# Kernel optimization log

Measured on AMD Instinct MI355X. Metric: run time of the kernel, lower is better.

The kernel has to match this reference:

```python
import jax, jax.numpy as jnp
import numpy as np

B, N, E, H = 16, 512, 256, 8
ALPHA = 0.2  # leaky relu negative slope


def setup_inputs() -> dict:
    key = jax.random.key(0)
    k1, k2, k3, k4, k5, k6 = jax.random.split(key, 6)
    x = jax.random.normal(k1, (B, N, E), dtype=jnp.float32)
    A = (jax.random.uniform(k2, (B, N, N)) < 0.3).astype(jnp.float32)
    s = 1.0 / np.sqrt(E)
    W = jax.random.uniform(k3, (E, E), minval=-s, maxval=s, dtype=jnp.float32)
    bW = jax.random.uniform(k4, (E,), minval=-s, maxval=s, dtype=jnp.float32)
    a = jax.random.uniform(k5, (E, 2 * H), minval=-s, maxval=s, dtype=jnp.float32)
    ba = jax.random.uniform(k6, (2 * H,), minval=-s, maxval=s, dtype=jnp.float32)
    return {"x": x, "A": A, "W": W, "bW": bW, "a": a, "ba": ba}


def reference(x, A, W, bW, a, ba):
    # Wh = W(x): [B, N, E]
    Wh = jnp.einsum("bne,ef->bnf", x, W) + bW
    # attention coefficients: a(Wh) -> [B, N, 2H] -> [B, H, N, 2]
    e12 = (jnp.einsum("bne,eh->bnh", Wh, a) + ba).reshape(B, N, H, 2).transpose(0, 2, 1, 3)
    e = e12[..., 0:1] + jnp.swapaxes(e12[..., 1:2], -2, -1)  # [B, H, N, N]
    # split heads: [B, H, N, D]
    Whh = Wh.reshape(B, N, H, E // H).transpose(0, 2, 1, 3)
    mask = A[:, None, :, :] > 0.5  # [B, H(bcast), N, N]
    neg = jnp.finfo(e.dtype).min
    score = jnp.where(mask, jax.nn.leaky_relu(e, ALPHA), neg)
    att = jax.nn.softmax(score, axis=-1)
    # rows with no neighbors: torch softmax(-inf row) -> nan -> nan_to_num -> 0
    has_nbr = jnp.any(mask, axis=-1, keepdims=True)
    att = jnp.where(has_nbr, att, 0.0)
    out = jnp.einsum("bhij,bhjd->bhid", att, Whh)  # [B, H, N, D]
    out = out.transpose(0, 2, 1, 3).reshape(B, N, E)
    # dropout is identity in eval/reference mode
    return jax.nn.relu(out)
```

## Files before the change

kernel.cpp:

```cpp
#include <hip/hip_runtime.h>
#include <math.h>

#define Bv 16
#define Nv 512
#define Ev 256
#define Hv 8
#define Dv 32
#define LOG2E 1.44269504088896340736f

typedef _Float16 half8 __attribute__((ext_vector_type(8)));
typedef _Float16 half4_t __attribute__((ext_vector_type(4)));
typedef float f32x4 __attribute__((ext_vector_type(4)));

__global__ __launch_bounds__(256) void fused_pre(const float* __restrict__ x,
                                                 const float* __restrict__ W,
                                                 const float* __restrict__ bW,
                                                 const float* __restrict__ aP,
                                                 const float* __restrict__ ba,
                                                 const float* __restrict__ A,
                                                 _Float16* __restrict__ WhT,
                                                 float* __restrict__ Wa,
                                                 float* __restrict__ cba,
                                                 unsigned int* __restrict__ Abm) {
    __shared__ _Float16 Wp[64][264];
    __shared__ _Float16 xs[64][40];
    __shared__ _Float16 ldsTr[64][72];

    const int tid = threadIdx.x;
    const int blk = blockIdx.x;

    if (blk < 512) {
        const int m0 = (blk >> 2) * 64;
        const int n0 = (blk & 3) * 64;
        const int w = tid >> 6;
        const int lane = tid & 63;
        const int row = lane & 15;
        const int strip = lane >> 4;

        {
            const float* wrow = &W[(size_t)tid * Ev + n0];
            #pragma unroll
            for (int u = 0; u < 16; ++u) {
                float4 v = *(const float4*)&wrow[u * 4];
                Wp[u * 4 + 0][tid] = (_Float16)v.x;
                Wp[u * 4 + 1][tid] = (_Float16)v.y;
                Wp[u * 4 + 2][tid] = (_Float16)v.z;
                Wp[u * 4 + 3][tid] = (_Float16)v.w;
            }
        }

        f32x4 acc[4] = {{0.f, 0.f, 0.f, 0.f}, {0.f, 0.f, 0.f, 0.f},
                        {0.f, 0.f, 0.f, 0.f}, {0.f, 0.f, 0.f, 0.f}};
        const int sr = tid >> 2;
        const int skg = (tid & 3) * 8;

        for (int k0 = 0; k0 < Ev; k0 += 32) {
            {
                const float* xp = &x[(size_t)(m0 + sr) * Ev + k0 + skg];
                float4 v0 = *(const float4*)xp;
                float4 v1 = *(const float4*)(xp + 4);
                half8 hv;
                hv[0] = (_Float16)v0.x; hv[1] = (_Float16)v0.y;
                hv[2] = (_Float16)v0.z; hv[3] = (_Float16)v0.w;
                hv[4] = (_Float16)v1.x; hv[5] = (_Float16)v1.y;
                hv[6] = (_Float16)v1.z; hv[7] = (_Float16)v1.w;
                *(half8*)&xs[sr][skg] = hv;
            }
            __syncthreads();

            half8 af = *(const half8*)&xs[w * 16 + row][strip * 8];
            #pragma unroll
            for (int ns = 0; ns < 4; ++ns) {
                half8 bf = *(const half8*)&Wp[ns * 16 + row][k0 + strip * 8];
                acc[ns] = __builtin_amdgcn_mfma_f32_16x16x32_f16(af, bf, acc[ns], 0, 0, 0);
            }
            __syncthreads();
        }

        #pragma unroll
        for (int ns = 0; ns < 4; ++ns) {
            const float bias = bW[n0 + ns * 16 + row];
            half4_t hv;
            hv[0] = (_Float16)(acc[ns][0] + bias);
            hv[1] = (_Float16)(acc[ns][1] + bias);
            hv[2] = (_Float16)(acc[ns][2] + bias);
            hv[3] = (_Float16)(acc[ns][3] + bias);
            *(half4_t*)&ldsTr[ns * 16 + row][w * 16 + strip * 4] = hv;
        }
        __syncthreads();

        {
            const int n = tid >> 2, jg = tid & 3;
            uint4 v0 = *(const uint4*)&ldsTr[n][jg * 16];
            uint4 v1 = *(const uint4*)&ldsTr[n][jg * 16 + 8];
            const int ng = n0 + n;
            const int h = ng >> 5, d = ng & 31;
            const int b = m0 >> 9, j0 = m0 & 511;
            _Float16* dst = &WhT[(((size_t)b * Hv + h) * Dv + d) * Nv + j0 + jg * 16];
            *(uint4*)dst = v0;
            *(uint4*)(dst + 8) = v1;
        }
    } else if (blk < 528) {
        const int e = (blk - 512) * 16 + (tid >> 4);
        const int c = tid & 15;
        float dot = 0.f;
        for (int k4 = 0; k4 < 64; ++k4) {
            float4 wv = *(const float4*)&W[(size_t)e * Ev + k4 * 4];
            dot += wv.x * aP[(k4 * 4 + 0) * 16 + c];
            dot += wv.y * aP[(k4 * 4 + 1) * 16 + c];
            dot += wv.z * aP[(k4 * 4 + 2) * 16 + c];
            dot += wv.w * aP[(k4 * 4 + 3) * 16 + c];
        }
        Wa[e * 16 + c] = dot;
    } else if (blk == 528) {
        if (tid < 16) {
            float d = ba[tid];
            for (int k = 0; k < Ev; ++k) d += bW[k] * aP[k * 16 + tid];
            cba[tid] = d;
        }
    } else {
        const int ablk = blk - 529;
        const int w = tid >> 6, lane = tid & 63;
        const size_t base = (size_t)ablk * 2048 + w * 512;
        #pragma unroll
        for (int r = 0; r < 8; ++r) {
            const size_t f = base + r * 64 + lane;
            const bool pred = A[f] > 0.5f;
            unsigned long long m = __ballot(pred);
            if (lane == 0) *(unsigned long long*)&Abm[f >> 5] = m;
        }
    }
}

__global__ __launch_bounds__(256) void e12_kernel(const float* __restrict__ x,
                                                  const float* __restrict__ Wa,
                                                  const float* __restrict__ cba,
                                                  float* __restrict__ e1,
                                                  float* __restrict__ e2) {
    __shared__ float WaS[Ev][16];
    __shared__ float cbaS[16];

    const int tid = threadIdx.x;
    const int m0 = blockIdx.x * 32;

    #pragma unroll
    for (int u = 0; u < 4; ++u) {
        int f = tid + u * 256;
        *(float4*)&WaS[f >> 2][(f & 3) * 4] = *(const float4*)&Wa[f * 4];
    }
    if (tid < 16) cbaS[tid] = cba[tid];
    __syncthreads();

    const int r = tid >> 3;
    const int q = (tid >> 1) & 3;
    const int kh = tid & 1;
    const int m = m0 + r;

    const float* xr = &x[(size_t)m * Ev + kh * 128];
    float4 acc = {0.f, 0.f, 0.f, 0.f};

    #pragma unroll 8
    for (int it = 0; it < 32; ++it) {
        float4 xv = *(const float4*)&xr[it * 4];
        const int kb = kh * 128 + it * 4;
        float4 w0 = *(const float4*)&WaS[kb + 0][q * 4];
        float4 w1 = *(const float4*)&WaS[kb + 1][q * 4];
        float4 w2 = *(const float4*)&WaS[kb + 2][q * 4];
        float4 w3 = *(const float4*)&WaS[kb + 3][q * 4];
        acc.x += xv.x * w0.x + xv.y * w1.x + xv.z * w2.x + xv.w * w3.x;
        acc.y += xv.x * w0.y + xv.y * w1.y + xv.z * w2.y + xv.w * w3.y;
        acc.z += xv.x * w0.z + xv.y * w1.z + xv.z * w2.z + xv.w * w3.z;
        acc.w += xv.x * w0.w + xv.y * w1.w + xv.z * w2.w + xv.w * w3.w;
    }

    acc.x += __shfl_xor(acc.x, 1);
    acc.y += __shfl_xor(acc.y, 1);
    acc.z += __shfl_xor(acc.z, 1);
    acc.w += __shfl_xor(acc.w, 1);

    if (kh == 0) {
        const int b = m >> 9, i = m & 511;
        #pragma unroll
        for (int cc = 0; cc < 4; ++cc) {
            const int c = q * 4 + cc;
            const float val = ((cc == 0) ? acc.x : (cc == 1) ? acc.y : (cc == 2) ? acc.z : acc.w)
                              + cbaS[c];
            const int h = c >> 1;
            float* dst = (c & 1) ? e2 : e1;
            dst[(((b << 3) + h) << 9) + i] = val;
        }
    }
}

__global__ __launch_bounds__(256) void attn_kernel(const unsigned int* __restrict__ Abm,
                                                   const _Float16* __restrict__ WhT,
                                                   const float* __restrict__ e1g,
                                                   const float* __restrict__ e2g,
                                                   float* __restrict__ out) {
    __shared__ _Float16 whT[Dv * Nv];
    __shared__ float E2pS[Nv];
    __shared__ float E2nS[Nv];

    const int tid = threadIdx.x;
    const int i0 = blockIdx.x * 128;
    const int h = blockIdx.y;
    const int b = blockIdx.z;
    const int bh = (b << 3) + h;

    const _Float16* src = WhT + (size_t)bh * (Dv * Nv);
    #pragma unroll
    for (int u = 0; u < 8; ++u) {
        int f = tid + u * 256;
        int d = f >> 6, bq = f & 63;
        uint4 v = *(const uint4*)(src + d * Nv + bq * 8);
        *(uint4*)&whT[d * Nv + ((bq ^ (d & 7)) * 8)] = v;
    }
    {
        float ea = e2g[(bh << 9) + tid] * LOG2E;
        E2pS[tid] = __builtin_amdgcn_exp2f(ea);
        E2nS[tid] = __builtin_amdgcn_exp2f(0.2f * ea);
        float eb = e2g[(bh << 9) + tid + 256] * LOG2E;
        E2pS[tid + 256] = __builtin_amdgcn_exp2f(eb);
        E2nS[tid + 256] = __builtin_amdgcn_exp2f(0.2f * eb);
    }
    __syncthreads();

    const int w = tid >> 6;
    const int lane = tid & 63;
    const int row = lane & 15;
    const int strip = lane >> 4;
    const int iA = i0 + (w << 5) + row;
    const int iB = iA + 16;

    const float e1A = e1g[(bh << 9) + iA] * LOG2E;
    const float e1B = e1g[(bh << 9) + iB] * LOG2E;
    const float E1pA = __builtin_amdgcn_exp2f(e1A);
    const float E1nA = __builtin_amdgcn_exp2f(0.2f * e1A);
    const float E1pB = __builtin_amdgcn_exp2f(e1B);
    const float E1nB = __builtin_amdgcn_exp2f(0.2f * e1B);

    const uint4* bpA = (const uint4*)&Abm[((size_t)b * Nv + iA) << 4];
    const uint4 mA0 = bpA[0], mA1 = bpA[1], mA2 = bpA[2], mA3 = bpA[3];
    const uint4* bpB = (const uint4*)&Abm[((size_t)b * Nv + iB) << 4];
    const uint4 mB0 = bpB[0], mB1 = bpB[1], mB2 = bpB[2], mB3 = bpB[3];

    const int sh = strip << 3;
    const int d0 = lane & 15;
    const int sw = d0 & 7;
    const _Float16* brow0 = &whT[d0 * Nv];
    const _Float16* brow1 = &whT[(16 + d0) * Nv];

    f32x4 accA0 = {0.f, 0.f, 0.f, 0.f}, accA1 = accA0;
    f32x4 accB0 = accA0, accB1 = accA0;
    float denA = 0.f, denB = 0.f;

    #pragma unroll
    for (int t = 0; t < 16; ++t) {
        const uint4 mqA = (t >> 2) == 0 ? mA0 : (t >> 2) == 1 ? mA1 : (t >> 2) == 2 ? mA2 : mA3;
        const uint4 mqB = (t >> 2) == 0 ? mB0 : (t >> 2) == 1 ? mB1 : (t >> 2) == 2 ? mB2 : mB3;
        const unsigned int dwA = (t & 3) == 0 ? mqA.x : (t & 3) == 1 ? mqA.y : (t & 3) == 2 ? mqA.z : mqA.w;
        const unsigned int dwB = (t & 3) == 0 ? mqB.x : (t & 3) == 1 ? mqB.y : (t & 3) == 2 ? mqB.z : mqB.w;
        const unsigned int byA = (dwA >> sh) & 0xFFu;
        const unsigned int byB = (dwB >> sh) & 0xFFu;

        const float4 p0 = *(const float4*)&E2pS[t * 32 + sh];
        const float4 p1 = *(const float4*)&E2pS[t * 32 + sh + 4];
        const float4 n0 = *(const float4*)&E2nS[t * 32 + sh];
        const float4 n1 = *(const float4*)&E2nS[t * 32 + sh + 4];

        const float qA0 = (byA & 1u)   ? fmaxf(E1pA * p0.x, E1nA * n0.x) : 0.f;
        const float qA1 = (byA & 2u)   ? fmaxf(E1pA * p0.y, E1nA * n0.y) : 0.f;
        const float qA2 = (byA & 4u)   ? fmaxf(E1pA * p0.z, E1nA * n0.z) : 0.f;
        const float qA3 = (byA & 8u)   ? fmaxf(E1pA * p0.w, E1nA * n0.w) : 0.f;
        const float qA4 = (byA & 16u)  ? fmaxf(E1pA * p1.x, E1nA * n1.x) : 0.f;
        const float qA5 = (byA & 32u)  ? fmaxf(E1pA * p1.y, E1nA * n1.y) : 0.f;
        const float qA6 = (byA & 64u)  ? fmaxf(E1pA * p1.z, E1nA * n1.z) : 0.f;
        const float qA7 = (byA & 128u) ? fmaxf(E1pA * p1.w, E1nA * n1.w) : 0.f;
        const float qB0 = (byB & 1u)   ? fmaxf(E1pB * p0.x, E1nB * n0.x) : 0.f;
        const float qB1 = (byB & 2u)   ? fmaxf(E1pB * p0.y, E1nB * n0.y) : 0.f;
        const float qB2 = (byB & 4u)   ? fmaxf(E1pB * p0.z, E1nB * n0.z) : 0.f;
        const float qB3 = (byB & 8u)   ? fmaxf(E1pB * p0.w, E1nB * n0.w) : 0.f;
        const float qB4 = (byB & 16u)  ? fmaxf(E1pB * p1.x, E1nB * n1.x) : 0.f;
        const float qB5 = (byB & 32u)  ? fmaxf(E1pB * p1.y, E1nB * n1.y) : 0.f;
        const float qB6 = (byB & 64u)  ? fmaxf(E1pB * p1.z, E1nB * n1.z) : 0.f;
        const float qB7 = (byB & 128u) ? fmaxf(E1pB * p1.w, E1nB * n1.w) : 0.f;

        denA += ((qA0 + qA1) + (qA2 + qA3)) + ((qA4 + qA5) + (qA6 + qA7));
        denB += ((qB0 + qB1) + (qB2 + qB3)) + ((qB4 + qB5) + (qB6 + qB7));

        half8 afA, afB;
        afA[0] = (_Float16)qA0; afA[1] = (_Float16)qA1;
        afA[2] = (_Float16)qA2; afA[3] = (_Float16)qA3;
        afA[4] = (_Float16)qA4; afA[5] = (_Float16)qA5;
        afA[6] = (_Float16)qA6; afA[7] = (_Float16)qA7;
        afB[0] = (_Float16)qB0; afB[1] = (_Float16)qB1;
        afB[2] = (_Float16)qB2; afB[3] = (_Float16)qB3;
        afB[4] = (_Float16)qB4; afB[5] = (_Float16)qB5;
        afB[6] = (_Float16)qB6; afB[7] = (_Float16)qB7;

        const int bq = ((t << 2) + strip) ^ sw;
        half8 b0 = *(const half8*)(brow0 + bq * 8);
        half8 b1 = *(const half8*)(brow1 + bq * 8);
        accA0 = __builtin_amdgcn_mfma_f32_16x16x32_f16(afA, b0, accA0, 0, 0, 0);
        accA1 = __builtin_amdgcn_mfma_f32_16x16x32_f16(afA, b1, accA1, 0, 0, 0);
        accB0 = __builtin_amdgcn_mfma_f32_16x16x32_f16(afB, b0, accB0, 0, 0, 0);
        accB1 = __builtin_amdgcn_mfma_f32_16x16x32_f16(afB, b1, accB1, 0, 0, 0);
    }

    denA += __shfl_xor(denA, 16);
    denA += __shfl_xor(denA, 32);
    denB += __shfl_xor(denB, 16);
    denB += __shfl_xor(denB, 32);

    #pragma unroll
    for (int e = 0; e < 4; ++e) {
        const float dnA = __shfl(denA, (strip << 2) + e);
        const float rvA = (dnA > 0.f) ? (1.f / dnA) : 0.f;
        const int orA = i0 + (w << 5) + (strip << 2) + e;
        float* opA = &out[((size_t)b * Nv + orA) * Ev + (h << 5)];
        opA[d0] = fmaxf(accA0[e] * rvA, 0.f);
        opA[16 + d0] = fmaxf(accA1[e] * rvA, 0.f);

        const float dnB = __shfl(denB, (strip << 2) + e);
        const float rvB = (dnB > 0.f) ? (1.f / dnB) : 0.f;
        const int orB = orA + 16;
        float* opB = &out[((size_t)b * Nv + orB) * Ev + (h << 5)];
        opB[d0] = fmaxf(accB0[e] * rvB, 0.f);
        opB[16 + d0] = fmaxf(accB1[e] * rvB, 0.f);
    }
}

extern "C" void kernel_launch(void* const* d_in, const int* in_sizes, int n_in,
                              void* d_out, int out_size, void* d_ws, size_t ws_size,
                              hipStream_t stream) {
    const float* x  = (const float*)d_in[0];
    const float* A  = (const float*)d_in[1];
    const float* W  = (const float*)d_in[2];
    const float* bW = (const float*)d_in[3];
    const float* a  = (const float*)d_in[4];
    const float* ba = (const float*)d_in[5];
    float* out = (float*)d_out;

    char* ws = (char*)d_ws;
    float*        Wa  = (float*)(ws);
    float*        cba = (float*)(ws + 16384);
    float*        e1  = (float*)(ws + 32768);
    float*        e2  = (float*)(ws + 294912);
    unsigned int* Abm = (unsigned int*)(ws + 557056);
    _Float16*     WhT = (_Float16*)(ws + 1572864);

    fused_pre<<<2577, 256, 0, stream>>>(x, W, bW, a, ba, A, WhT, Wa, cba, Abm);
    e12_kernel<<<dim3(Bv * Nv / 32), 256, 0, stream>>>(x, Wa, cba, e1, e2);
    attn_kernel<<<dim3(Nv / 128, Hv, Bv), 256, 0, stream>>>(Abm, WhT, e1, e2, out);
}
```

Baseline: 42.75 us.

## Use MFMA for attention logits, double-buffer x tile, pack fp16 converts

```diff
diff --git a/kernel.cpp b/kernel.cpp
--- a/kernel.cpp
+++ b/kernel.cpp
@@ -10,6 +10,7 @@
 
 typedef _Float16 half8 __attribute__((ext_vector_type(8)));
 typedef _Float16 half4_t __attribute__((ext_vector_type(4)));
+typedef __fp16 fp16x2 __attribute__((ext_vector_type(2)));
 typedef float f32x4 __attribute__((ext_vector_type(4)));
 
 __global__ __launch_bounds__(256) void fused_pre(const float* __restrict__ x,
@@ -19,11 +20,11 @@
                                                  const float* __restrict__ ba,
                                                  const float* __restrict__ A,
                                                  _Float16* __restrict__ WhT,
-                                                 float* __restrict__ Wa,
+                                                 _Float16* __restrict__ WaT,
                                                  float* __restrict__ cba,
                                                  unsigned int* __restrict__ Abm) {
     __shared__ _Float16 Wp[64][264];
-    __shared__ _Float16 xs[64][40];
+    __shared__ _Float16 xs[2][64][40];
     __shared__ _Float16 ldsTr[64][72];
 
     const int tid = threadIdx.x;
@@ -49,32 +50,51 @@
             }
         }
 
+        const int sr = tid >> 2;
+        const int skg = (tid & 3) * 8;
+        const float* xrow = &x[(size_t)(m0 + sr) * Ev + skg];
+
+        {
+            float4 v0 = *(const float4*)xrow;
+            float4 v1 = *(const float4*)(xrow + 4);
+            half8 hv;
+            hv[0] = (_Float16)v0.x; hv[1] = (_Float16)v0.y;
+            hv[2] = (_Float16)v0.z; hv[3] = (_Float16)v0.w;
+            hv[4] = (_Float16)v1.x; hv[5] = (_Float16)v1.y;
+            hv[6] = (_Float16)v1.z; hv[7] = (_Float16)v1.w;
+            *(half8*)&xs[0][sr][skg] = hv;
+        }
+        __syncthreads();
+
         f32x4 acc[4] = {{0.f, 0.f, 0.f, 0.f}, {0.f, 0.f, 0.f, 0.f},
                         {0.f, 0.f, 0.f, 0.f}, {0.f, 0.f, 0.f, 0.f}};
-        const int sr = tid >> 2;
-        const int skg = (tid & 3) * 8;
-
-        for (int k0 = 0; k0 < Ev; k0 += 32) {
-            {
-                const float* xp = &x[(size_t)(m0 + sr) * Ev + k0 + skg];
-                float4 v0 = *(const float4*)xp;
-                float4 v1 = *(const float4*)(xp + 4);
-                half8 hv;
-                hv[0] = (_Float16)v0.x; hv[1] = (_Float16)v0.y;
-                hv[2] = (_Float16)v0.z; hv[3] = (_Float16)v0.w;
-                hv[4] = (_Float16)v1.x; hv[5] = (_Float16)v1.y;
-                hv[6] = (_Float16)v1.z; hv[7] = (_Float16)v1.w;
-                *(half8*)&xs[sr][skg] = hv;
+        int cur = 0;
+
+        #pragma unroll
+        for (int it = 0; it < 8; ++it) {
+            float4 nv0, nv1;
+            if (it < 7) {
+                nv0 = *(const float4*)(xrow + (it + 1) * 32);
+                nv1 = *(const float4*)(xrow + (it + 1) * 32 + 4);
             }
-            __syncthreads();
-
-            half8 af = *(const half8*)&xs[w * 16 + row][strip * 8];
+
+            half8 af = *(const half8*)&xs[cur][w * 16 + row][strip * 8];
             #pragma unroll
             for (int ns = 0; ns < 4; ++ns) {
-                half8 bf = *(const half8*)&Wp[ns * 16 + row][k0 + strip * 8];
+                half8 bf = *(const half8*)&Wp[ns * 16 + row][it * 32 + strip * 8];
                 acc[ns] = __builtin_amdgcn_mfma_f32_16x16x32_f16(af, bf, acc[ns], 0, 0, 0);
             }
-            __syncthreads();
+
+            if (it < 7) {
+                half8 hv;
+                hv[0] = (_Float16)nv0.x; hv[1] = (_Float16)nv0.y;
+                hv[2] = (_Float16)nv0.z; hv[3] = (_Float16)nv0.w;
+                hv[4] = (_Float16)nv1.x; hv[5] = (_Float16)nv1.y;
+                hv[6] = (_Float16)nv1.z; hv[7] = (_Float16)nv1.w;
+                *(half8*)&xs[cur ^ 1][sr][skg] = hv;
+                __syncthreads();
+                cur ^= 1;
+            }
         }
 
         #pragma unroll
@@ -111,7 +131,7 @@
             dot += wv.z * aP[(k4 * 4 + 2) * 16 + c];
             dot += wv.w * aP[(k4 * 4 + 3) * 16 + c];
         }
-        Wa[e * 16 + c] = dot;
+        WaT[(size_t)c * Ev + e] = (_Float16)dot;
     } else if (blk == 528) {
         if (tid < 16) {
             float d = ba[tid];
@@ -132,63 +152,47 @@
     }
 }
 
-__global__ __launch_bounds__(256) void e12_kernel(const float* __restrict__ x,
-                                                  const float* __restrict__ Wa,
-                                                  const float* __restrict__ cba,
-                                                  float* __restrict__ e1,
-                                                  float* __restrict__ e2) {
-    __shared__ float WaS[Ev][16];
-    __shared__ float cbaS[16];
-
-    const int tid = threadIdx.x;
-    const int m0 = blockIdx.x * 32;
-
-    #pragma unroll
-    for (int u = 0; u < 4; ++u) {
-        int f = tid + u * 256;
-        *(float4*)&WaS[f >> 2][(f & 3) * 4] = *(const float4*)&Wa[f * 4];
-    }
-    if (tid < 16) cbaS[tid] = cba[tid];
-    __syncthreads();
-
-    const int r = tid >> 3;
-    const int q = (tid >> 1) & 3;
-    const int kh = tid & 1;
-    const int m = m0 + r;
-
-    const float* xr = &x[(size_t)m * Ev + kh * 128];
-    float4 acc = {0.f, 0.f, 0.f, 0.f};
-
-    #pragma unroll 8
-    for (int it = 0; it < 32; ++it) {
-        float4 xv = *(const float4*)&xr[it * 4];
-        const int kb = kh * 128 + it * 4;
-        float4 w0 = *(const float4*)&WaS[kb + 0][q * 4];
-        float4 w1 = *(const float4*)&WaS[kb + 1][q * 4];
-        float4 w2 = *(const float4*)&WaS[kb + 2][q * 4];
-        float4 w3 = *(const float4*)&WaS[kb + 3][q * 4];
-        acc.x += xv.x * w0.x + xv.y * w1.x + xv.z * w2.x + xv.w * w3.x;
-        acc.y += xv.x * w0.y + xv.y * w1.y + xv.z * w2.y + xv.w * w3.y;
-        acc.z += xv.x * w0.z + xv.y * w1.z + xv.z * w2.z + xv.w * w3.z;
-        acc.w += xv.x * w0.w + xv.y * w1.w + xv.z * w2.w + xv.w * w3.w;
-    }
-
-    acc.x += __shfl_xor(acc.x, 1);
-    acc.y += __shfl_xor(acc.y, 1);
-    acc.z += __shfl_xor(acc.z, 1);
-    acc.w += __shfl_xor(acc.w, 1);
-
-    if (kh == 0) {
+__global__ __launch_bounds__(64) void e12_mfma(const float* __restrict__ x,
+                                               const _Float16* __restrict__ WaT,
+                                               const float* __restrict__ cba,
+                                               float* __restrict__ e1,
+                                               float* __restrict__ e2) {
+    const int lane = threadIdx.x;
+    const int m0 = blockIdx.x * 16;
+    const int l15 = lane & 15;
+    const int strip = lane >> 4;
+
+    const float* xr = &x[(size_t)(m0 + l15) * Ev + strip * 8];
+    const _Float16* wr = &WaT[(size_t)l15 * Ev + strip * 8];
+
+    f32x4 acc = {0.f, 0.f, 0.f, 0.f};
+    #pragma unroll
+    for (int kt = 0; kt < 8; ++kt) {
+        float4 a0 = *(const float4*)&xr[kt * 32];
+        float4 a1 = *(const float4*)&xr[kt * 32 + 4];
+        fp16x2 h0 = __builtin_amdgcn_cvt_pkrtz(a0.x, a0.y);
+        fp16x2 h1 = __builtin_amdgcn_cvt_pkrtz(a0.z, a0.w);
+        fp16x2 h2 = __builtin_amdgcn_cvt_pkrtz(a1.x, a1.y);
+        fp16x2 h3 = __builtin_amdgcn_cvt_pkrtz(a1.z, a1.w);
+        uint4 U;
+        U.x = __builtin_bit_cast(unsigned int, h0);
+        U.y = __builtin_bit_cast(unsigned int, h1);
+        U.z = __builtin_bit_cast(unsigned int, h2);
+        U.w = __builtin_bit_cast(unsigned int, h3);
+        half8 af = __builtin_bit_cast(half8, U);
+        half8 bf = *(const half8*)&wr[kt * 32];
+        acc = __builtin_amdgcn_mfma_f32_16x16x32_f16(af, bf, acc, 0, 0, 0);
+    }
+
+    const int c = l15;
+    const float cb = cba[c];
+    const int h = c >> 1;
+    float* dst = (c & 1) ? e2 : e1;
+    #pragma unroll
+    for (int e = 0; e < 4; ++e) {
+        const int m = m0 + strip * 4 + e;
         const int b = m >> 9, i = m & 511;
-        #pragma unroll
-        for (int cc = 0; cc < 4; ++cc) {
-            const int c = q * 4 + cc;
-            const float val = ((cc == 0) ? acc.x : (cc == 1) ? acc.y : (cc == 2) ? acc.z : acc.w)
-                              + cbaS[c];
-            const int h = c >> 1;
-            float* dst = (c & 1) ? e2 : e1;
-            dst[(((b << 3) + h) << 9) + i] = val;
-        }
+        dst[(((b << 3) + h) << 9) + i] = acc[e] + cb;
     }
 }
 
@@ -288,15 +292,26 @@
         denA += ((qA0 + qA1) + (qA2 + qA3)) + ((qA4 + qA5) + (qA6 + qA7));
         denB += ((qB0 + qB1) + (qB2 + qB3)) + ((qB4 + qB5) + (qB6 + qB7));
 
-        half8 afA, afB;
-        afA[0] = (_Float16)qA0; afA[1] = (_Float16)qA1;
-        afA[2] = (_Float16)qA2; afA[3] = (_Float16)qA3;
-        afA[4] = (_Float16)qA4; afA[5] = (_Float16)qA5;
-        afA[6] = (_Float16)qA6; afA[7] = (_Float16)qA7;
-        afB[0] = (_Float16)qB0; afB[1] = (_Float16)qB1;
-        afB[2] = (_Float16)qB2; afB[3] = (_Float16)qB3;
-        afB[4] = (_Float16)qB4; afB[5] = (_Float16)qB5;
-        afB[6] = (_Float16)qB6; afB[7] = (_Float16)qB7;
+        fp16x2 a01 = __builtin_amdgcn_cvt_pkrtz(qA0, qA1);
+        fp16x2 a23 = __builtin_amdgcn_cvt_pkrtz(qA2, qA3);
+        fp16x2 a45 = __builtin_amdgcn_cvt_pkrtz(qA4, qA5);
+        fp16x2 a67 = __builtin_amdgcn_cvt_pkrtz(qA6, qA7);
+        fp16x2 b01 = __builtin_amdgcn_cvt_pkrtz(qB0, qB1);
+        fp16x2 b23 = __builtin_amdgcn_cvt_pkrtz(qB2, qB3);
+        fp16x2 b45 = __builtin_amdgcn_cvt_pkrtz(qB4, qB5);
+        fp16x2 b67 = __builtin_amdgcn_cvt_pkrtz(qB6, qB7);
+
+        uint4 UA, UB;
+        UA.x = __builtin_bit_cast(unsigned int, a01);
+        UA.y = __builtin_bit_cast(unsigned int, a23);
+        UA.z = __builtin_bit_cast(unsigned int, a45);
+        UA.w = __builtin_bit_cast(unsigned int, a67);
+        UB.x = __builtin_bit_cast(unsigned int, b01);
+        UB.y = __builtin_bit_cast(unsigned int, b23);
+        UB.z = __builtin_bit_cast(unsigned int, b45);
+        UB.w = __builtin_bit_cast(unsigned int, b67);
+        half8 afA = __builtin_bit_cast(half8, UA);
+        half8 afB = __builtin_bit_cast(half8, UB);
 
         const int bq = ((t << 2) + strip) ^ sw;
         half8 b0 = *(const half8*)(brow0 + bq * 8);
@@ -342,14 +357,14 @@
     float* out = (float*)d_out;
 
     char* ws = (char*)d_ws;
-    float*        Wa  = (float*)(ws);
+    _Float16*     WaT = (_Float16*)(ws);
     float*        cba = (float*)(ws + 16384);
     float*        e1  = (float*)(ws + 32768);
     float*        e2  = (float*)(ws + 294912);
     unsigned int* Abm = (unsigned int*)(ws + 557056);
     _Float16*     WhT = (_Float16*)(ws + 1572864);
 
-    fused_pre<<<2577, 256, 0, stream>>>(x, W, bW, a, ba, A, WhT, Wa, cba, Abm);
-    e12_kernel<<<dim3(Bv * Nv / 32), 256, 0, stream>>>(x, Wa, cba, e1, e2);
+    fused_pre<<<2577, 256, 0, stream>>>(x, W, bW, a, ba, A, WhT, WaT, cba, Abm);
+    e12_mfma<<<Bv * Nv / 16, 64, 0, stream>>>(x, WaT, cba, e1, e2);
     attn_kernel<<<dim3(Nv / 128, Hv, Bv), 256, 0, stream>>>(Abm, WhT, e1, e2, out);
 }
```

After: 41.88 us. 1.02x faster.
